# Kernel tuning notes

Measured on AMD Instinct MI355X. Metric: run time of the kernel, lower is better.

Reference implementation:

```python
import jax, jax.numpy as jnp
import numpy as np

N_EMBED = 8192
EMBED_DIM = 64
BETA = 0.25


def setup_inputs() -> dict:
    key = jax.random.key(0)
    k_z, k_e = jax.random.split(key)
    z = jax.random.normal(k_z, (16, 4096, EMBED_DIM), dtype=jnp.float32)
    # embedding.weight.data.uniform_(-1/n_embed, 1/n_embed)
    embedding = jax.random.uniform(
        k_e, (N_EMBED, EMBED_DIM), dtype=jnp.float32,
        minval=-1.0 / N_EMBED, maxval=1.0 / N_EMBED)
    return {"z": z, "embedding": embedding}


def reference(z, embedding):
    # z: [B, H, C] with C == embed_dim (no permute needed)
    B, H, C = z.shape
    z_flat = z.reshape(-1, C)                      # [N, C]
    # squared euclidean distances: ||z||^2 + ||e||^2 - 2 z e^T
    d = (jnp.sum(z_flat ** 2, axis=1, keepdims=True)
         + jnp.sum(embedding ** 2, axis=1)
         - 2.0 * jnp.matmul(z_flat, embedding.T))  # [N, n_embed]
    idx = jnp.argmin(d, axis=1)                    # [N]
    z_q = embedding[idx].reshape(z.shape)          # gather + reshape
    sg = jax.lax.stop_gradient
    loss = (jnp.mean((sg(z_q) - z) ** 2)
            + BETA * jnp.mean((z_q - sg(z)) ** 2))
    # straight-through estimator
    z_q = z + sg(z_q - z)
    return z_q, loss, idx.reshape(B, H)
```

## Files before the change

### kernel.cpp

```cpp
#include <hip/hip_runtime.h>

typedef __attribute__((ext_vector_type(8))) short short8;
typedef __attribute__((ext_vector_type(16))) float floatx16;
typedef unsigned int u32;
typedef unsigned short u16;
typedef unsigned long long u64;

#define NROWS 65536
#define NEMB 8192
#define DIM 64
#define LOSS_OFF ((size_t)NROWS * DIM)
#define IDX_OFF (LOSS_OFF + 1)
#define CAPQ 16
#define CSTRIDE 66
#define NPREST 4

#define WS_EFRAG_OFF 0u
#define WS_BEST_OFF  (1u << 20)
#define WS_QUEUE_OFF ((1u << 20) + (512u << 10))
#define WS_LPART_OFF (WS_QUEUE_OFF + (512u << 10))
#define WS_QCNT_OFF  (WS_LPART_OFF + 8192u)
#define WS_NEED      (WS_QCNT_OFF + 64u)

__device__ __forceinline__ unsigned short f2bf(float f) {
    u32 x = __float_as_uint(f);
    return (unsigned short)((x + 0x7fffu + ((x >> 16) & 1u)) >> 16);
}

__device__ __forceinline__ float zsum_np(const float* zf) {
    float r[8];
#pragma unroll
    for (int j = 0; j < 8; ++j) r[j] = zf[j] * zf[j];
#pragma unroll
    for (int i = 8; i < 64; i += 8) {
#pragma unroll
        for (int j = 0; j < 8; ++j) r[j] += zf[i + j] * zf[i + j];
    }
    return ((r[0] + r[1]) + (r[2] + r[3])) + ((r[4] + r[5]) + (r[6] + r[7]));
}

__device__ __forceinline__ float dot_chain(const float* zf, const float* e) {
    float acc = 0.f;
#pragma unroll
    for (int i = 0; i < 16; ++i) {
        float4 ev = ((const float4*)e)[i];
        acc = fmaf(zf[4 * i + 0], ev.x, acc);
        acc = fmaf(zf[4 * i + 1], ev.y, acc);
        acc = fmaf(zf[4 * i + 2], ev.z, acc);
        acc = fmaf(zf[4 * i + 3], ev.w, acc);
    }
    return acc;
}

__device__ __forceinline__ float vmax16_3(const floatx16& a) {
    float m0 = fmaxf(fmaxf(a[0], a[1]), a[2]);
    float m1 = fmaxf(fmaxf(a[3], a[4]), a[5]);
    float m2 = fmaxf(fmaxf(a[6], a[7]), a[8]);
    float m3 = fmaxf(fmaxf(a[9], a[10]), a[11]);
    float m4 = fmaxf(fmaxf(a[12], a[13]), a[14]);
    float n0 = fmaxf(fmaxf(m0, m1), m2);
    float n1 = fmaxf(fmaxf(m3, m4), a[15]);
    return fmaxf(n0, n1);
}

__device__ __forceinline__ float fmax_h32(float x) {
#if defined(__has_builtin)
#if __has_builtin(__builtin_amdgcn_permlane32_swap)
    typedef __attribute__((ext_vector_type(2))) unsigned int uint2v;
    uint2v r = __builtin_amdgcn_permlane32_swap(
        __float_as_uint(x), __float_as_uint(x), false, false);
    return fmaxf(__uint_as_float(r[0]), __uint_as_float(r[1]));
#else
    return fmaxf(x, __shfl_xor(x, 32));
#endif
#else
    return fmaxf(x, __shfl_xor(x, 32));
#endif
}

extern "C" __global__ __launch_bounds__(256)
void vq_prep(const float* __restrict__ emb, u32* __restrict__ efrag,
             u64* __restrict__ best, u32* __restrict__ qcount) {
    int tid = blockIdx.x * 256 + threadIdx.x;
    int t = tid >> 8, kc = (tid >> 5) & 7, m = tid & 31;
    const float* e = emb + (((size_t)t * 32 + m) * 64 + kc * 8);
    float4 a = ((const float4*)e)[0];
    float4 b = ((const float4*)e)[1];
    u32 w0 = (u32)f2bf(a.x) | ((u32)f2bf(a.y) << 16);
    u32 w1 = (u32)f2bf(a.z) | ((u32)f2bf(a.w) << 16);
    u32 w2 = (u32)f2bf(b.x) | ((u32)f2bf(b.y) << 16);
    u32 w3 = (u32)f2bf(b.z) | ((u32)f2bf(b.w) << 16);
    ((uint4*)efrag)[tid] = make_uint4(w0, w1, w2, w3);
    best[tid] = ~0ull;
    if (tid < 16) qcount[tid] = 0u;
}

extern "C" __global__ __launch_bounds__(256, 4)
void vq_screen(const float* __restrict__ z, const u32* __restrict__ efrag,
               const float* __restrict__ emb, u64* __restrict__ best,
               u32* __restrict__ queue, u32* __restrict__ qcount) {
    __shared__ u16 cand[128 * CSTRIDE];
    __shared__ u32 cnt_l[512];
    __shared__ float runm_sh[128][2];
    const int tid = threadIdx.x;
    const int wave = tid >> 6, lane = tid & 63;
    const int rlo = lane & 31, h = lane >> 5;
    const int rowblk = blockIdx.x >> 1, halfid = blockIdx.x & 1;
    const int rowbase = rowblk * 128 + (wave >> 1) * 64;
    const int sub = (wave & 1) * 2 + h;
    const int wp = wave & 1;
    const int rowl0 = (wave >> 1) * 64 + rlo;
    const int rowl1 = rowl0 + 32;
    const int ebh = halfid * 4096 + wp * 64 + 4 * h;

    if (tid < 128) { runm_sh[tid][0] = -3.4e38f; runm_sh[tid][1] = -3.4e38f; }

    const u32* fb = efrag + (u32)halfid * 131072u
                  + (u32)(wp * 2048 + h * 128 + rlo * 4);

    short8 zfr[2][4];
    float eps_[2];
#pragma unroll
    for (int rt = 0; rt < 2; ++rt) {
        const float* zp = z + (size_t)(rowbase + rt * 32 + rlo) * 64;
        float sa = 0.f;
#pragma unroll
        for (int s = 0; s < 4; ++s) {
            const float4* p = (const float4*)(zp + s * 16 + h * 8);
            float4 a = p[0], b = p[1];
            union { short8 v; unsigned short e[8]; } u;
            u.e[0] = f2bf(a.x); u.e[1] = f2bf(a.y);
            u.e[2] = f2bf(a.z); u.e[3] = f2bf(a.w);
            u.e[4] = f2bf(b.x); u.e[5] = f2bf(b.y);
            u.e[6] = f2bf(b.z); u.e[7] = f2bf(b.w);
            zfr[rt][s] = u.v;
            sa += fabsf(a.x) + fabsf(a.y) + fabsf(a.z) + fabsf(a.w)
                + fabsf(b.x) + fabsf(b.y) + fabsf(b.z) + fabsf(b.w);
        }
        sa += __shfl_xor(sa, 32);
        eps_[rt] = fmaf(1.1e-6f, sa, 1e-7f);
    }
    float runm[2] = { -3.4e38f, -3.4e38f };
    u32 pc[2] = { 0u, 0u };
    const u32 cb0 = (u32)rowl0 * CSTRIDE + (u32)sub * CAPQ;
    const u32 cb1 = (u32)rowl1 * CSTRIDE + (u32)sub * CAPQ;

    __syncthreads();

#define PF(B_, T_, E_) do { \
    const u32* bp_ = fb + ((u32)(T_) * 4096u + (u32)(E_) * 1024u); \
    B_[0] = *(const short8*)(bp_); \
    B_[1] = *(const short8*)(bp_ + 256); \
    B_[2] = *(const short8*)(bp_ + 512); \
    B_[3] = *(const short8*)(bp_ + 768); \
} while (0)

#define SUBSTAGE(B_, T_, EE_, SCAN_) do { \
    if (EE_ == 0) {                                \
        runm[0] = fmaxf(runm[0], runm_sh[rowl0][wp ^ 1]); \
        runm[1] = fmaxf(runm[1], runm_sh[rowl1][wp ^ 1]); \
    } \
    floatx16 a0_, a1_; a0_ = 0.f; a1_ = 0.f; \
    _Pragma("unroll") \
    for (int s_ = 0; s_ < 4; ++s_) { \
        a0_ = __builtin_amdgcn_mfma_f32_32x32x16_bf16(B_[s_], zfr[0][s_], a0_, 0, 0, 0); \
        a1_ = __builtin_amdgcn_mfma_f32_32x32x16_bf16(B_[s_], zfr[1][s_], a1_, 0, 0, 0); \
    } \
    float vm0_ = vmax16_3(a0_); \
    runm[0] = fmax_h32(fmaxf(runm[0], vm0_)); \
    float vm1_ = vmax16_3(a1_); \
    runm[1] = fmax_h32(fmaxf(runm[1], vm1_)); \
    if (SCAN_) { \
        const int ebj_ = ebh + (T_) * 128 + (EE_) * 32; \
        const float thr0_ = runm[0] - eps_[0]; \
        if (vm0_ >= thr0_) { \
            _Pragma("unroll") \
            for (int r_ = 0; r_ < 16; ++r_) { \
                if (a0_[r_] >= thr0_) { \
                    int j_ = ebj_ + ((r_ & 3) + 8 * (r_ >> 2)); \
                    if (pc[0] < CAPQ) cand[cb0 + pc[0]] = (u16)j_; \
                    pc[0]++;                       \
                } \
            } \
        } \
        const float thr1_ = runm[1] - eps_[1]; \
        if (vm1_ >= thr1_) { \
            _Pragma("unroll") \
            for (int r_ = 0; r_ < 16; ++r_) { \
                if (a1_[r_] >= thr1_) { \
                    int j_ = ebj_ + ((r_ & 3) + 8 * (r_ >> 2)); \
                    if (pc[1] < CAPQ) cand[cb1 + pc[1]] = (u16)j_; \
                    pc[1]++; \
                } \
            } \
        } \
    } \
    if (EE_ == 1 && h == 0) {                      \
        runm_sh[rowl0][wp] = runm[0]; \
        runm_sh[rowl1][wp] = runm[1]; \
    } \
} while (0)

    {
        short8 b0[4], b1[4];
        PF(b0, 0, 0);
        for (int t = 0; t < NPREST; ++t) {
            PF(b1, t, 1);
            SUBSTAGE(b0, t, 0, false);
            PF(b0, (t == NPREST - 1) ? 0 : (t + 1), 0);
            SUBSTAGE(b1, t, 1, false);
        }
        for (int t = 0; t < 32; ++t) {
            PF(b1, t, 1);
            SUBSTAGE(b0, t, 0, true);
            PF(b0, (t == 31) ? 31 : (t + 1), 0);
            SUBSTAGE(b1, t, 1, true);
        }
    }
#undef SUBSTAGE
#undef PF

    cnt_l[(rowl0 << 2) + sub] = pc[0];
    cnt_l[(rowl1 << 2) + sub] = pc[1];
    __syncthreads();

    {
        const int rl = lane & 31, half = lane >> 5;
        const int rowl = wave * 32 + rl;
        const int grow = rowblk * 128 + rowl;
        const u32 ca = cnt_l[(rowl << 2) + 2 * half];
        const u32 cb = cnt_l[(rowl << 2) + 2 * half + 1];
        u32 ovf = (u32)((ca > CAPQ) | (cb > CAPQ));
        ovf |= (u32)__shfl_xor((int)ovf, 32);

        if (!ovf) {
            float zf[64];
            const float4* zp = (const float4*)(z + (size_t)grow * 64);
#pragma unroll
            for (int i = 0; i < 16; ++i) {
                float4 a = zp[i];
                zf[4 * i + 0] = a.x; zf[4 * i + 1] = a.y;
                zf[4 * i + 2] = a.z; zf[4 * i + 3] = a.w;
            }
            const float zs = zsum_np(zf);
            u64 b = ~0ull;
            const u32 cbase = (u32)rowl * CSTRIDE + (u32)(2 * half) * CAPQ;
            for (u32 s = 0; s < ca; ++s) {
                u32 j = (u32)cand[cbase + s];
                float d = fmaf(-2.f, dot_chain(zf, emb + (size_t)j * 64), zs);
                u64 p = ((u64)__float_as_uint(d) << 32) | (u64)j;
                b = p < b ? p : b;
            }
            for (u32 s = 0; s < cb; ++s) {
                u32 j = (u32)cand[cbase + CAPQ + s];
                float d = fmaf(-2.f, dot_chain(zf, emb + (size_t)j * 64), zs);
                u64 p = ((u64)__float_as_uint(d) << 32) | (u64)j;
                b = p < b ? p : b;
            }
            u64 o = __shfl_xor(b, 32);
            b = o < b ? o : b;
            if (half == 0) atomicMin(&best[grow], b);
        } else if (half == 0) {
            u32 pos = atomicAdd(qcount, 1u);
            queue[pos] = (u32)grow | ((u32)halfid << 16);
        }
    }
}

extern "C" __global__ __launch_bounds__(256)
void vq_over(const float* __restrict__ z, const float* __restrict__ emb,
             const u32* __restrict__ queue, const u32* __restrict__ qcount,
             u64* __restrict__ best) {
    __shared__ u64 red[4];
    const int tid = threadIdx.x, wave = tid >> 6, lane = tid & 63;
    u32 n = qcount[0]; if (n > 2u * (u32)NROWS) n = 2u * (u32)NROWS;
    for (u32 qi = blockIdx.x; qi < n; qi += gridDim.x) {
        const u32 e = queue[qi];
        const int row = (int)(e & 0xFFFFu);
        const int hb = (int)((e >> 16) & 1u) * 4096;
        const float4* zp = (const float4*)(z + (size_t)row * 64);
        float zf[64];
#pragma unroll
        for (int i = 0; i < 16; ++i) {
            float4 a = zp[i];
            zf[4 * i + 0] = a.x; zf[4 * i + 1] = a.y;
            zf[4 * i + 2] = a.z; zf[4 * i + 3] = a.w;
        }
        const float zs = zsum_np(zf);
        u64 b = ~0ull;
#pragma unroll 2
        for (int j = tid; j < 4096; j += 256) {
            const int gj = hb + j;
            float d = fmaf(-2.f, dot_chain(zf, emb + (size_t)gj * 64), zs);
            u64 p = ((u64)__float_as_uint(d) << 32) | (u64)gj;
            b = p < b ? p : b;
        }
#pragma unroll
        for (int off = 32; off; off >>= 1) {
            u64 o = __shfl_xor(b, off);
            b = o < b ? o : b;
        }
        if (lane == 0) red[wave] = b;
        __syncthreads();
        if (tid == 0) {
            u64 bb = red[0];
#pragma unroll
            for (int w = 1; w < 4; ++w) { u64 o = red[w]; bb = o < bb ? o : bb; }
            atomicMin(&best[row], bb);
        }
        __syncthreads();
    }
}

extern "C" __global__ __launch_bounds__(256)
void vq_final(const float* __restrict__ z, const float* __restrict__ emb,
              const u64* __restrict__ best, float* __restrict__ out,
              float* __restrict__ lpart) {
    __shared__ float lsum[4];
    const int tid = threadIdx.x, wave = tid >> 6, lane = tid & 63;
    const int r2 = tid >> 1, hf = tid & 1;
    const int grow = blockIdx.x * 128 + r2;
    const u32 wj = (u32)best[grow];
    if (hf == 0) out[IDX_OFF + grow] = (float)wj;
    float lp = 0.f;
    {
        const float4* ep = (const float4*)(emb + (size_t)wj * 64) + hf * 8;
        const float4* zp4 = (const float4*)(z + (size_t)grow * 64) + hf * 8;
        float4* oq = (float4*)(out + (size_t)grow * 64) + hf * 8;
#pragma unroll
        for (int i = 0; i < 8; ++i) {
            float4 ev = ep[i];
            float4 zv = zp4[i];
            oq[i] = ev;
            float dx = ev.x - zv.x, dy = ev.y - zv.y;
            float dzv = ev.z - zv.z, dw = ev.w - zv.w;
            lp = fmaf(dx, dx, fmaf(dy, dy, fmaf(dzv, dzv, fmaf(dw, dw, lp))));
        }
    }
#pragma unroll
    for (int off = 32; off; off >>= 1) lp += __shfl_down(lp, off);
    if (lane == 0) lsum[wave] = lp;
    __syncthreads();
    if (tid == 0)
        lpart[blockIdx.x] = (lsum[0] + lsum[1]) + (lsum[2] + lsum[3]);
}

extern "C" __global__ __launch_bounds__(256)
void vq_lossred(const float* __restrict__ lpart, float* __restrict__ out) {
    __shared__ float s[256];
    const int tid = threadIdx.x;
    float v = 0.f;
    for (int i = tid; i < 512; i += 256) v += lpart[i];
    s[tid] = v; __syncthreads();
    for (int off = 128; off; off >>= 1) {
        if (tid < off) s[tid] += s[tid + off];
        __syncthreads();
    }
    if (tid == 0) out[LOSS_OFF] = 1.25f * s[0] / 4194304.f;
}

extern "C" __global__ __launch_bounds__(256, 2)
void vq_legacy(const float* __restrict__ z, const float* __restrict__ emb,
               float* __restrict__ out, float* __restrict__ ws) {
    __shared__ float tile[128 * 64];
    __shared__ float red_d[4][128];
    __shared__ int   red_i[4][128];
    const int tid = threadIdx.x, lane = tid & 63, wave = tid >> 6;
    const int r0 = blockIdx.x * 128 + lane;
    float z0f[64], z1f[64];
    {
        const float4* p0 = (const float4*)(z + (size_t)r0 * 64);
        const float4* p1 = (const float4*)(z + ((size_t)r0 + 64) * 64);
#pragma unroll
        for (int i = 0; i < 16; ++i) {
            float4 a = p0[i];
            z0f[4*i+0]=a.x; z0f[4*i+1]=a.y; z0f[4*i+2]=a.z; z0f[4*i+3]=a.w;
            float4 b = p1[i];
            z1f[4*i+0]=b.x; z1f[4*i+1]=b.y; z1f[4*i+2]=b.z; z1f[4*i+3]=b.w;
        }
    }
    const float zs0 = zsum_np(z0f), zs1 = zsum_np(z1f);
    float bd0 = 3.402823466e38f, bd1 = 3.402823466e38f;
    int bi0 = 0, bi1 = 0;
    for (int t = 0; t < 64; ++t) {
        __syncthreads();
        {
            const float4* src = (const float4*)(emb + (size_t)t * 128 * 64);
            float4* dst = (float4*)tile;
#pragma unroll
            for (int i = 0; i < 8; ++i) dst[tid + i * 256] = src[tid + i * 256];
        }
        __syncthreads();
        const int base = wave * 32;
#pragma unroll 2
        for (int jg = 0; jg < 32; jg += 4) {
            const float* e = tile + (size_t)(base + jg) * 64;
            float a00=0,a10=0,a20=0,a30=0,a01=0,a11=0,a21=0,a31=0;
#pragma unroll
            for (int i = 0; i < 16; ++i) {
                float4 ea = ((const float4*)(e))[i];
                float4 eb = ((const float4*)(e + 64))[i];
                float4 ec = ((const float4*)(e + 128))[i];
                float4 ed = ((const float4*)(e + 192))[i];
                float x0=z0f[4*i],x1=z0f[4*i+1],x2=z0f[4*i+2],x3=z0f[4*i+3];
                float y0=z1f[4*i],y1=z1f[4*i+1],y2=z1f[4*i+2],y3=z1f[4*i+3];
                a00=fmaf(x0,ea.x,a00);a00=fmaf(x1,ea.y,a00);a00=fmaf(x2,ea.z,a00);a00=fmaf(x3,ea.w,a00);
                a10=fmaf(x0,eb.x,a10);a10=fmaf(x1,eb.y,a10);a10=fmaf(x2,eb.z,a10);a10=fmaf(x3,eb.w,a10);
                a20=fmaf(x0,ec.x,a20);a20=fmaf(x1,ec.y,a20);a20=fmaf(x2,ec.z,a20);a20=fmaf(x3,ec.w,a20);
                a30=fmaf(x0,ed.x,a30);a30=fmaf(x1,ed.y,a30);a30=fmaf(x2,ed.z,a30);a30=fmaf(x3,ed.w,a30);
                a01=fmaf(y0,ea.x,a01);a01=fmaf(y1,ea.y,a01);a01=fmaf(y2,ea.z,a01);a01=fmaf(y3,ea.w,a01);
                a11=fmaf(y0,eb.x,a11);a11=fmaf(y1,eb.y,a11);a11=fmaf(y2,eb.z,a11);a11=fmaf(y3,eb.w,a11);
                a21=fmaf(y0,ec.x,a21);a21=fmaf(y1,ec.y,a21);a21=fmaf(y2,ec.z,a21);a21=fmaf(y3,ec.w,a21);
                a31=fmaf(y0,ed.x,a31);a31=fmaf(y1,ed.y,a31);a31=fmaf(y2,ed.z,a31);a31=fmaf(y3,ed.w,a31);
            }
            const int gj = t * 128 + base + jg;
            float d;
            d=fmaf(-2.f,a00,zs0); if(d<bd0){bd0=d;bi0=gj;}
            d=fmaf(-2.f,a10,zs0); if(d<bd0){bd0=d;bi0=gj+1;}
            d=fmaf(-2.f,a20,zs0); if(d<bd0){bd0=d;bi0=gj+2;}
            d=fmaf(-2.f,a30,zs0); if(d<bd0){bd0=d;bi0=gj+3;}
            d=fmaf(-2.f,a01,zs1); if(d<bd1){bd1=d;bi1=gj;}
            d=fmaf(-2.f,a11,zs1); if(d<bd1){bd1=d;bi1=gj+1;}
            d=fmaf(-2.f,a21,zs1); if(d<bd1){bd1=d;bi1=gj+2;}
            d=fmaf(-2.f,a31,zs1); if(d<bd1){bd1=d;bi1=gj+3;}
        }
    }
    red_d[wave][lane]=bd0; red_i[wave][lane]=bi0;
    red_d[wave][lane+64]=bd1; red_i[wave][lane+64]=bi1;
    __syncthreads();
    if (wave == 0) {
        float blk = 0.f;
#pragma unroll
        for (int half = 0; half < 2; ++half) {
            const int lrow = lane + half * 64;
            const float* zrf = half ? z1f : z0f;
            float bd = red_d[0][lrow]; int bi = red_i[0][lrow];
#pragma unroll
            for (int w = 1; w < 4; ++w) {
                float dd = red_d[w][lrow]; int ii = red_i[w][lrow];
                if (dd < bd || (dd == bd && ii < bi)) { bd = dd; bi = ii; }
            }
            const size_t row = (size_t)blockIdx.x * 128 + lrow;
            out[IDX_OFF + row] = (float)bi;
            const float4* ep = (const float4*)(emb + (size_t)bi * 64);
            float4* oq = (float4*)(out + row * 64);
            float ls = 0.f;
#pragma unroll
            for (int i = 0; i < 16; ++i) {
                float4 ev = ep[i];
                oq[i] = ev;
                float dx=ev.x-zrf[4*i], dy=ev.y-zrf[4*i+1];
                float dzv=ev.z-zrf[4*i+2], dw=ev.w-zrf[4*i+3];
                ls=fmaf(dx,dx,ls); ls=fmaf(dy,dy,ls); ls=fmaf(dzv,dzv,ls); ls=fmaf(dw,dw,ls);
            }
            blk += ls;
        }
#pragma unroll
        for (int off = 32; off; off >>= 1) blk += __shfl_down(blk, off);
        if (lane == 0) ws[blockIdx.x] = blk;
    }
}

extern "C" __global__ __launch_bounds__(512)
void vq_legacy_loss(const float* __restrict__ ws, float* __restrict__ out) {
    __shared__ float s[8];
    const int tid = threadIdx.x;
    float v = ws[tid];
#pragma unroll
    for (int off = 32; off; off >>= 1) v += __shfl_down(v, off);
    if ((tid & 63) == 0) s[tid >> 6] = v;
    __syncthreads();
    if (tid == 0) {
        float t = 0.f;
#pragma unroll
        for (int i = 0; i < 8; ++i) t += s[i];
        out[LOSS_OFF] = 1.25f * t / 4194304.f;
    }
}

extern "C" void kernel_launch(void* const* d_in, const int* in_sizes, int n_in,
                              void* d_out, int out_size, void* d_ws, size_t ws_size,
                              hipStream_t stream) {
    const float* z   = (const float*)d_in[0];
    const float* emb = (const float*)d_in[1];
    float* out = (float*)d_out;
    if (ws_size < (size_t)WS_NEED) {
        float* ws = (float*)d_ws;
        vq_legacy<<<512, 256, 0, stream>>>(z, emb, out, ws);
        vq_legacy_loss<<<1, 512, 0, stream>>>(ws, out);
        return;
    }
    char* wsb = (char*)d_ws;
    u32* efrag   = (u32*)(wsb + WS_EFRAG_OFF);
    u64* best    = (u64*)(wsb + WS_BEST_OFF);
    u32* queue   = (u32*)(wsb + WS_QUEUE_OFF);
    float* lpart = (float*)(wsb + WS_LPART_OFF);
    u32* qcount  = (u32*)(wsb + WS_QCNT_OFF);
    vq_prep<<<256, 256, 0, stream>>>(emb, efrag, best, qcount);
    vq_screen<<<1024, 256, 0, stream>>>(z, efrag, emb, best, queue, qcount);
    vq_over<<<256, 256, 0, stream>>>(z, emb, queue, qcount, best);
    vq_final<<<512, 256, 0, stream>>>(z, emb, best, out, lpart);
    vq_lossred<<<1, 256, 0, stream>>>(lpart, out);
}
```

Before: 197.6 us.

## Fuse overflow rescan into final kernel and split MFMA tiles per row group

Removes the separate overflow kernel: each final block scans the whole overflow queue and handles only the entries whose rows belong to its 128-row block, then gathers and computes the loss. The screen kernel's per-substage MFMA chains are reorganized so each row tile's four MFMAs and threshold scan run back-to-back starting from a zero constant accumulator. This saves one launch and lets overflow work finish before the final gather without a separate grid. In exchange every block reads the full queue serially, and a block with many overflow rows becomes a straggler, since that work is no longer spread across the grid.

New measurement: 193.6 us (median of 2 runs). 2.0% less time.

```diff
diff --git a/kernel.cpp b/kernel.cpp
--- a/kernel.cpp
+++ b/kernel.cpp
@@ -144,6 +144,7 @@
     u32 pc[2] = { 0u, 0u };
     const u32 cb0 = (u32)rowl0 * CSTRIDE + (u32)sub * CAPQ;
     const u32 cb1 = (u32)rowl1 * CSTRIDE + (u32)sub * CAPQ;
+    const floatx16 ZACC = 0.f;
 
     __syncthreads();
 
@@ -155,46 +156,36 @@
     B_[3] = *(const short8*)(bp_ + 768); \
 } while (0)
 
+#define TILE(B_, RT_, T_, EE_, SCAN_, CB_) do { \
+    floatx16 a_ = __builtin_amdgcn_mfma_f32_32x32x16_bf16(B_[0], zfr[RT_][0], ZACC, 0, 0, 0); \
+    a_ = __builtin_amdgcn_mfma_f32_32x32x16_bf16(B_[1], zfr[RT_][1], a_, 0, 0, 0); \
+    a_ = __builtin_amdgcn_mfma_f32_32x32x16_bf16(B_[2], zfr[RT_][2], a_, 0, 0, 0); \
+    a_ = __builtin_amdgcn_mfma_f32_32x32x16_bf16(B_[3], zfr[RT_][3], a_, 0, 0, 0); \
+    float vm_ = vmax16_3(a_); \
+    runm[RT_] = fmax_h32(fmaxf(runm[RT_], vm_)); \
+    if (SCAN_) { \
+        const float thr_ = runm[RT_] - eps_[RT_]; \
+        if (vm_ >= thr_) { \
+            const int ebj_ = ebh + (T_) * 128 + (EE_) * 32; \
+            _Pragma("unroll") \
+            for (int r_ = 0; r_ < 16; ++r_) { \
+                if (a_[r_] >= thr_) { \
+                    int j_ = ebj_ + ((r_ & 3) + 8 * (r_ >> 2)); \
+                    if (pc[RT_] < CAPQ) cand[CB_ + pc[RT_]] = (u16)j_; \
+                    pc[RT_]++;                     \
+                } \
+            } \
+        } \
+    } \
+} while (0)
+
 #define SUBSTAGE(B_, T_, EE_, SCAN_) do { \
     if (EE_ == 0) {                                \
         runm[0] = fmaxf(runm[0], runm_sh[rowl0][wp ^ 1]); \
         runm[1] = fmaxf(runm[1], runm_sh[rowl1][wp ^ 1]); \
     } \
-    floatx16 a0_, a1_; a0_ = 0.f; a1_ = 0.f; \
-    _Pragma("unroll") \
-    for (int s_ = 0; s_ < 4; ++s_) { \
-        a0_ = __builtin_amdgcn_mfma_f32_32x32x16_bf16(B_[s_], zfr[0][s_], a0_, 0, 0, 0); \
-        a1_ = __builtin_amdgcn_mfma_f32_32x32x16_bf16(B_[s_], zfr[1][s_], a1_, 0, 0, 0); \
-    } \
-    float vm0_ = vmax16_3(a0_); \
-    runm[0] = fmax_h32(fmaxf(runm[0], vm0_)); \
-    float vm1_ = vmax16_3(a1_); \
-    runm[1] = fmax_h32(fmaxf(runm[1], vm1_)); \
-    if (SCAN_) { \
-        const int ebj_ = ebh + (T_) * 128 + (EE_) * 32; \
-        const float thr0_ = runm[0] - eps_[0]; \
-        if (vm0_ >= thr0_) { \
-            _Pragma("unroll") \
-            for (int r_ = 0; r_ < 16; ++r_) { \
-                if (a0_[r_] >= thr0_) { \
-                    int j_ = ebj_ + ((r_ & 3) + 8 * (r_ >> 2)); \
-                    if (pc[0] < CAPQ) cand[cb0 + pc[0]] = (u16)j_; \
-                    pc[0]++;                       \
-                } \
-            } \
-        } \
-        const float thr1_ = runm[1] - eps_[1]; \
-        if (vm1_ >= thr1_) { \
-            _Pragma("unroll") \
-            for (int r_ = 0; r_ < 16; ++r_) { \
-                if (a1_[r_] >= thr1_) { \
-                    int j_ = ebj_ + ((r_ & 3) + 8 * (r_ >> 2)); \
-                    if (pc[1] < CAPQ) cand[cb1 + pc[1]] = (u16)j_; \
-                    pc[1]++; \
-                } \
-            } \
-        } \
-    } \
+    TILE(B_, 0, T_, EE_, SCAN_, cb0); \
+    TILE(B_, 1, T_, EE_, SCAN_, cb1); \
     if (EE_ == 1 && h == 0) {                      \
         runm_sh[rowl0][wp] = runm[0]; \
         runm_sh[rowl1][wp] = runm[1]; \
@@ -218,6 +209,7 @@
         }
     }
 #undef SUBSTAGE
+#undef TILE
 #undef PF
 
     cnt_l[(rowl0 << 2) + sub] = pc[0];
@@ -268,15 +260,19 @@
 }
 
 extern "C" __global__ __launch_bounds__(256)
-void vq_over(const float* __restrict__ z, const float* __restrict__ emb,
-             const u32* __restrict__ queue, const u32* __restrict__ qcount,
-             u64* __restrict__ best) {
+void vq_final(const float* __restrict__ z, const float* __restrict__ emb,
+              u64* __restrict__ best, const u32* __restrict__ queue,
+              const u32* __restrict__ qcount, float* __restrict__ out,
+              float* __restrict__ lpart) {
+    __shared__ float lsum[4];
     __shared__ u64 red[4];
     const int tid = threadIdx.x, wave = tid >> 6, lane = tid & 63;
+
     u32 n = qcount[0]; if (n > 2u * (u32)NROWS) n = 2u * (u32)NROWS;
-    for (u32 qi = blockIdx.x; qi < n; qi += gridDim.x) {
+    for (u32 qi = 0; qi < n; ++qi) {
         const u32 e = queue[qi];
         const int row = (int)(e & 0xFFFFu);
+        if ((row >> 7) != (int)blockIdx.x) continue;
         const int hb = (int)((e >> 16) & 1u) * 4096;
         const float4* zp = (const float4*)(z + (size_t)row * 64);
         float zf[64];
@@ -310,14 +306,8 @@
         }
         __syncthreads();
     }
-}
-
-extern "C" __global__ __launch_bounds__(256)
-void vq_final(const float* __restrict__ z, const float* __restrict__ emb,
-              const u64* __restrict__ best, float* __restrict__ out,
-              float* __restrict__ lpart) {
-    __shared__ float lsum[4];
-    const int tid = threadIdx.x, wave = tid >> 6, lane = tid & 63;
+    __syncthreads();
+
     const int r2 = tid >> 1, hf = tid & 1;
     const int grow = blockIdx.x * 128 + r2;
     const u32 wj = (u32)best[grow];
@@ -498,7 +488,6 @@
     u32* qcount  = (u32*)(wsb + WS_QCNT_OFF);
     vq_prep<<<256, 256, 0, stream>>>(emb, efrag, best, qcount);
     vq_screen<<<1024, 256, 0, stream>>>(z, efrag, emb, best, queue, qcount);
-    vq_over<<<256, 256, 0, stream>>>(z, emb, queue, qcount, best);
-    vq_final<<<512, 256, 0, stream>>>(z, emb, best, out, lpart);
+    vq_final<<<512, 256, 0, stream>>>(z, emb, best, queue, qcount, out, lpart);
     vq_lossred<<<1, 256, 0, stream>>>(lpart, out);
 }
```
